# Performance work log

Hardware: AMD Instinct MI355X
Metric: run time of the kernel (lower is better)

## Reference

```python
import jax, jax.numpy as jnp
import numpy as np

N, E, H, L, G, MAX_Z = 100000, 1600000, 128, 3, 1024, 1000
BN_EPS = 1e-5

def setup_inputs() -> dict:
    key = jax.random.key(0)
    ks = jax.random.split(key, 16)
    z = jax.random.randint(ks[0], (N,), 0, MAX_Z)
    edge_index = jax.random.randint(ks[1], (2, E), 0, N)
    batch = jnp.sort(jax.random.randint(ks[2], (N,), 0, G))
    s = 1.0 / np.sqrt(H)
    z_table = jax.random.normal(ks[3], (MAX_Z, H), jnp.float32)
    conv_W1 = jax.random.normal(ks[4], (L, H, H), jnp.float32) * s
    conv_b1 = jnp.zeros((L, H), jnp.float32)
    conv_W2 = jax.random.normal(ks[5], (L, H, H), jnp.float32) * s
    conv_b2 = jnp.zeros((L, H), jnp.float32)
    bn_gamma = jnp.ones((L, H), jnp.float32)
    bn_beta = jnp.zeros((L, H), jnp.float32)
    lin1_W = jax.random.normal(ks[6], (L * H, H), jnp.float32) / np.sqrt(L * H)
    lin1_b = jnp.zeros((H,), jnp.float32)
    lin2_W = jax.random.normal(ks[7], (H, 1), jnp.float32) * s
    lin2_b = jnp.zeros((1,), jnp.float32)
    return {"z": z, "edge_index": edge_index, "batch": batch,
            "z_table": z_table, "conv_W1": conv_W1, "conv_b1": conv_b1,
            "conv_W2": conv_W2, "conv_b2": conv_b2, "bn_gamma": bn_gamma,
            "bn_beta": bn_beta, "lin1_W": lin1_W, "lin1_b": lin1_b,
            "lin2_W": lin2_W, "lin2_b": lin2_b}

def _gin_layer(x, src, dst, W1, b1, W2, b2, gamma, beta):
    # GIN sum aggregation: (1+eps)*x_i + sum_{j->i} x_j  (eps=0)
    agg = x + jax.ops.segment_sum(x[src], dst, num_segments=N)
    h = jax.nn.relu(agg @ W1 + b1)
    h = jax.nn.relu(h @ W2 + b2)
    # BatchNorm1d (training-mode batch statistics over nodes)
    mu = jnp.mean(h, axis=0)
    var = jnp.mean(jnp.square(h - mu), axis=0)
    return gamma * (h - mu) * jax.lax.rsqrt(var + BN_EPS) + beta

def reference(z, edge_index, batch, z_table, conv_W1, conv_b1, conv_W2,
              conv_b2, bn_gamma, bn_beta, lin1_W, lin1_b, lin2_W, lin2_b):
    src, dst = edge_index[0], edge_index[1]
    x = z_table[z]                      # [N, H]
    xs = []
    for l in range(L):
        x = _gin_layer(x, src, dst, conv_W1[l], conv_b1[l], conv_W2[l],
                       conv_b2[l], bn_gamma[l], bn_beta[l])
        xs.append(x)
    feat = jnp.concatenate(xs, axis=1)  # [N, L*H] (jk=True)
    sums = jax.ops.segment_sum(feat, batch, num_segments=G)
    cnt = jax.ops.segment_sum(jnp.ones((N,), feat.dtype), batch, num_segments=G)
    pooled = sums / jnp.maximum(cnt, 1.0)[:, None]   # global_mean_pool [G, L*H]
    h = jax.nn.relu(pooled @ lin1_W + lin1_b)
    # dropout inactive (eval mode)
    return h @ lin2_W + lin2_b          # [G, 1]
```

## Files before the change

### kernel.cpp

```cpp
#include <hip/hip_runtime.h>

#define NN 100000
#define NE 1600000
#define HD 128
#define NL 3
#define NG 1024
#define BN_EPS 1e-5f
#define SCAN_CHUNK 1024

static inline int cdiv(int a, int b) { return (a + b - 1) / b; }

__global__ __launch_bounds__(256) void embed_kernel(const int* __restrict__ z,
    const float* __restrict__ table, float* __restrict__ x) {
  int t = blockIdx.x * 256 + threadIdx.x;
  if (t >= NN * 32) return;
  int row = t >> 5, c4 = (t & 31) << 2;
  int zi = z[row];
  *(float4*)(x + (size_t)row * HD + c4) =
      *(const float4*)(table + (size_t)zi * HD + c4);
}

__global__ __launch_bounds__(256) void zero_counts_kernel(int* __restrict__ cnt) {
  int t = blockIdx.x * 256 + threadIdx.x;
  if (t < NN) cnt[t] = 0;
}

__global__ __launch_bounds__(256) void hist_kernel(const int* __restrict__ dstI,
    int* __restrict__ cnt) {
  int e = blockIdx.x * 256 + threadIdx.x;
  if (e < NE) atomicAdd(&cnt[dstI[e]], 1);
}

__global__ __launch_bounds__(256) void scan_block_kernel(const int* __restrict__ cnt,
    int* __restrict__ rowptr, int* __restrict__ bsums) {
  __shared__ int sh[SCAN_CHUNK];
  __shared__ int ts[256];
  int base = blockIdx.x * SCAN_CHUNK;
  for (int i = threadIdx.x; i < SCAN_CHUNK; i += 256)
    sh[i] = (base + i < NN) ? cnt[base + i] : 0;
  __syncthreads();
  int t4 = threadIdx.x * 4;
  int a0 = sh[t4], a1 = sh[t4 + 1], a2 = sh[t4 + 2], a3 = sh[t4 + 3];
  int tsum = a0 + a1 + a2 + a3;
  ts[threadIdx.x] = tsum;
  __syncthreads();
  for (int off = 1; off < 256; off <<= 1) {
    int v = ts[threadIdx.x];
    int u = (threadIdx.x >= off) ? ts[threadIdx.x - off] : 0;
    __syncthreads();
    ts[threadIdx.x] = v + u;
    __syncthreads();
  }
  int texcl = ts[threadIdx.x] - tsum;
  sh[t4] = texcl;
  sh[t4 + 1] = texcl + a0;
  sh[t4 + 2] = texcl + a0 + a1;
  sh[t4 + 3] = texcl + a0 + a1 + a2;
  __syncthreads();
  for (int i = threadIdx.x; i < SCAN_CHUNK; i += 256) {
    int g = base + i;
    if (g < NN) rowptr[g] = sh[i];
  }
  if (threadIdx.x == 255) bsums[blockIdx.x] = ts[255];
}

__global__ void scan_bsums_kernel(int* __restrict__ bsums, int nb) {
  if (threadIdx.x == 0) {
    int run = 0;
    for (int i = 0; i < nb; ++i) { int v = bsums[i]; bsums[i] = run; run += v; }
  }
}

__global__ __launch_bounds__(256) void scan_add_kernel(int* __restrict__ rowptr,
    const int* __restrict__ bsums, int* __restrict__ fill_off) {
  int t = blockIdx.x * 256 + threadIdx.x;
  if (t < NN) {
    int v = rowptr[t] + bsums[t / SCAN_CHUNK];
    rowptr[t] = v;
    fill_off[t] = v;
  }
  if (t == 0) rowptr[NN] = NE;
}

__global__ __launch_bounds__(256) void fill_kernel(const int* __restrict__ srcI,
    const int* __restrict__ dstI, int* __restrict__ fill_off, int* __restrict__ esrc) {
  int e = blockIdx.x * 256 + threadIdx.x;
  if (e >= NE) return;
  int d = dstI[e];
  int pos = atomicAdd(&fill_off[d], 1);
  esrc[pos] = srcI[e];
}

__global__ __launch_bounds__(256) void agg_kernel(const int* __restrict__ rowptr,
    const int* __restrict__ esrc, const float* __restrict__ xin, int xstride,
    float* __restrict__ agg) {
  int n = blockIdx.x * 4 + (threadIdx.x >> 6);
  if (n >= NN) return;
  int lane = threadIdx.x & 63;
  int lo = rowptr[n], hi = rowptr[n + 1];
  int deg = hi - lo;
  float2 acc = *(const float2*)(xin + (size_t)n * xstride + lane * 2);

  for (int base = 0; base < deg; base += 64) {
    int cnt = deg - base; if (cnt > 64) cnt = 64;
    int idx = (base + lane < deg) ? esrc[lo + base + lane] : 0;
    int j = 0;
    for (; j + 4 <= cnt; j += 4) {
      int s0 = __shfl(idx, j, 64);
      int s1 = __shfl(idx, j + 1, 64);
      int s2 = __shfl(idx, j + 2, 64);
      int s3 = __shfl(idx, j + 3, 64);
      float2 v0 = *(const float2*)(xin + (size_t)s0 * xstride + lane * 2);
      float2 v1 = *(const float2*)(xin + (size_t)s1 * xstride + lane * 2);
      float2 v2 = *(const float2*)(xin + (size_t)s2 * xstride + lane * 2);
      float2 v3 = *(const float2*)(xin + (size_t)s3 * xstride + lane * 2);
      acc.x += v0.x + v1.x + v2.x + v3.x;
      acc.y += v0.y + v1.y + v2.y + v3.y;
    }
    for (; j < cnt; ++j) {
      int s = __shfl(idx, j, 64);
      float2 v = *(const float2*)(xin + (size_t)s * xstride + lane * 2);
      acc.x += v.x; acc.y += v.y;
    }
  }
  *(float2*)(agg + (size_t)n * HD + lane * 2) = acc;
}

template <int STATS>
__global__ __launch_bounds__(256) void gemm_relu_kernel_t(
    const float* __restrict__ A, const float* __restrict__ B,
    const float* __restrict__ bias, float* __restrict__ C, int M,
    float* __restrict__ gsums) {
  __shared__ float As[128][65];
  __shared__ float Bs[32][128];
  __shared__ float csum[256];
  const int tid = threadIdx.x;
  const int row0 = blockIdx.x * 64;

  if (STATS) { csum[tid] = 0.f; }

  #pragma unroll
  for (int i = 0; i < 8; ++i) {
    int f = tid + i * 256;
    int row = f >> 5;
    int kq = (f & 31) << 2;
    int gr = row0 + row;
    float4 v = make_float4(0.f, 0.f, 0.f, 0.f);
    if (gr < M) v = *(const float4*)(A + (size_t)gr * HD + kq);
    As[kq + 0][row] = v.x; As[kq + 1][row] = v.y;
    As[kq + 2][row] = v.z; As[kq + 3][row] = v.w;
  }

  const int colbase = (tid & 15) << 2;
  const int rowbase = (tid >> 4) << 2;
  float acc[4][8] = {};

  for (int kc = 0; kc < 4; ++kc) {
    __syncthreads();
    #pragma unroll
    for (int i = 0; i < 4; ++i) {
      int f = tid + i * 256;
      int k = f >> 5;
      int c4 = (f & 31) << 2;
      *(float4*)(&Bs[k][c4]) = *(const float4*)(B + (size_t)(kc * 32 + k) * HD + c4);
    }
    __syncthreads();
    #pragma unroll
    for (int k = 0; k < 32; ++k) {
      const int kk = kc * 32 + k;
      float a0 = As[kk][rowbase + 0];
      float a1 = As[kk][rowbase + 1];
      float a2 = As[kk][rowbase + 2];
      float a3 = As[kk][rowbase + 3];
      float4 bl = *(const float4*)(&Bs[k][colbase]);
      float4 bh = *(const float4*)(&Bs[k][colbase + 64]);
      acc[0][0] += a0 * bl.x; acc[0][1] += a0 * bl.y; acc[0][2] += a0 * bl.z; acc[0][3] += a0 * bl.w;
      acc[0][4] += a0 * bh.x; acc[0][5] += a0 * bh.y; acc[0][6] += a0 * bh.z; acc[0][7] += a0 * bh.w;
      acc[1][0] += a1 * bl.x; acc[1][1] += a1 * bl.y; acc[1][2] += a1 * bl.z; acc[1][3] += a1 * bl.w;
      acc[1][4] += a1 * bh.x; acc[1][5] += a1 * bh.y; acc[1][6] += a1 * bh.z; acc[1][7] += a1 * bh.w;
      acc[2][0] += a2 * bl.x; acc[2][1] += a2 * bl.y; acc[2][2] += a2 * bl.z; acc[2][3] += a2 * bl.w;
      acc[2][4] += a2 * bh.x; acc[2][5] += a2 * bh.y; acc[2][6] += a2 * bh.z; acc[2][7] += a2 * bh.w;
      acc[3][0] += a3 * bl.x; acc[3][1] += a3 * bl.y; acc[3][2] += a3 * bl.z; acc[3][3] += a3 * bl.w;
      acc[3][4] += a3 * bh.x; acc[3][5] += a3 * bh.y; acc[3][6] += a3 * bh.z; acc[3][7] += a3 * bh.w;
    }
  }

  float4 bvl = *(const float4*)(bias + colbase);
  float4 bvh = *(const float4*)(bias + colbase + 64);
  float ps[8] = {}, pq[8] = {};
  #pragma unroll
  for (int r = 0; r < 4; ++r) {
    int gr = row0 + rowbase + r;
    if (gr < M) {
      float4 o;
      o.x = fmaxf(acc[r][0] + bvl.x, 0.f);
      o.y = fmaxf(acc[r][1] + bvl.y, 0.f);
      o.z = fmaxf(acc[r][2] + bvl.z, 0.f);
      o.w = fmaxf(acc[r][3] + bvl.w, 0.f);
      *(float4*)(C + (size_t)gr * HD + colbase) = o;
      if (STATS) {
        ps[0] += o.x; ps[1] += o.y; ps[2] += o.z; ps[3] += o.w;
        pq[0] += o.x * o.x; pq[1] += o.y * o.y; pq[2] += o.z * o.z; pq[3] += o.w * o.w;
      }
      o.x = fmaxf(acc[r][4] + bvh.x, 0.f);
      o.y = fmaxf(acc[r][5] + bvh.y, 0.f);
      o.z = fmaxf(acc[r][6] + bvh.z, 0.f);
      o.w = fmaxf(acc[r][7] + bvh.w, 0.f);
      *(float4*)(C + (size_t)gr * HD + colbase + 64) = o;
      if (STATS) {
        ps[4] += o.x; ps[5] += o.y; ps[6] += o.z; ps[7] += o.w;
        pq[4] += o.x * o.x; pq[5] += o.y * o.y; pq[6] += o.z * o.z; pq[7] += o.w * o.w;
      }
    }
  }

  if (STATS) {
    __syncthreads();
    #pragma unroll
    for (int c = 0; c < 4; ++c) {
      atomicAdd(&csum[colbase + c], ps[c]);
      atomicAdd(&csum[128 + colbase + c], pq[c]);
      atomicAdd(&csum[colbase + 64 + c], ps[4 + c]);
      atomicAdd(&csum[128 + colbase + 64 + c], pq[4 + c]);
    }
    __syncthreads();
    if (tid < 128) {
      atomicAdd(&gsums[tid], csum[tid]);
      atomicAdd(&gsums[HD + tid], csum[128 + tid]);
    }
  }
}

__global__ void zero_kernel(float* p) { p[threadIdx.x] = 0.f; }

__global__ void bn_finalize_kernel(const float* __restrict__ sums,
    const float* __restrict__ gamma, const float* __restrict__ beta,
    float* __restrict__ ss) {
  int c = threadIdx.x;
  float mu = sums[c] * (1.f / NN);
  float var = sums[HD + c] * (1.f / NN) - mu * mu;
  float sc = gamma[c] * rsqrtf(var + BN_EPS);
  ss[c] = sc;
  ss[HD + c] = beta[c] - mu * sc;
}

__global__ __launch_bounds__(256) void bn_apply_kernel(const float* __restrict__ h,
    const float* __restrict__ ss, float* __restrict__ featl) {
  int t = blockIdx.x * 256 + threadIdx.x;
  if (t >= NN * 32) return;
  int row = t >> 5, c4 = (t & 31) << 2;
  float4 v = *(const float4*)(h + (size_t)row * HD + c4);
  float4 sc = *(const float4*)(ss + c4);
  float4 sh = *(const float4*)(ss + HD + c4);
  float4 o;
  o.x = v.x * sc.x + sh.x;
  o.y = v.y * sc.y + sh.y;
  o.z = v.z * sc.z + sh.z;
  o.w = v.w * sc.w + sh.w;
  *(float4*)(featl + (size_t)row * (NL * HD) + c4) = o;
}

__device__ __forceinline__ int lbound(const int* __restrict__ b, int val) {
  int lo = 0, hi = NN;
  while (lo < hi) { int m = (lo + hi) >> 1; if (b[m] < val) lo = m + 1; else hi = m; }
  return lo;
}

__global__ __launch_bounds__(384) void pool_kernel(const int* __restrict__ batch,
    const float* __restrict__ feat, float* __restrict__ pooled) {
  int g = blockIdx.x;
  int lo = lbound(batch, g), hi = lbound(batch, g + 1);
  float s = 0.f;
  for (int r = lo; r < hi; ++r) s += feat[(size_t)r * (NL * HD) + threadIdx.x];
  float inv = 1.f / (float)max(hi - lo, 1);
  pooled[(size_t)g * (NL * HD) + threadIdx.x] = s * inv;
}

__global__ __launch_bounds__(128) void mlp_kernel(const float* __restrict__ pooled,
    const float* __restrict__ W1, const float* __restrict__ b1,
    const float* __restrict__ W2, const float* __restrict__ b2,
    float* __restrict__ out) {
  int g = blockIdx.x, c = threadIdx.x;
  const float* p = pooled + (size_t)g * (NL * HD);
  float acc = b1[c];
  #pragma unroll 4
  for (int k = 0; k < NL * HD; ++k) acc = fmaf(p[k], W1[(size_t)k * HD + c], acc);
  acc = fmaxf(acc, 0.f);
  float prod = acc * W2[c];
  #pragma unroll
  for (int off = 32; off > 0; off >>= 1) prod += __shfl_xor(prod, off, 64);
  __shared__ float part[2];
  if ((c & 63) == 0) part[c >> 6] = prod;
  __syncthreads();
  if (c == 0) out[g] = part[0] + part[1] + b2[0];
}

extern "C" void kernel_launch(void* const* d_in, const int* in_sizes, int n_in,
                              void* d_out, int out_size, void* d_ws, size_t ws_size,
                              hipStream_t stream) {
  (void)in_sizes; (void)n_in; (void)out_size; (void)ws_size;
  const int*   z     = (const int*)d_in[0];
  const int*   ei    = (const int*)d_in[1];
  const int*   batch = (const int*)d_in[2];
  const float* ztab  = (const float*)d_in[3];
  const float* W1    = (const float*)d_in[4];
  const float* b1    = (const float*)d_in[5];
  const float* W2    = (const float*)d_in[6];
  const float* b2    = (const float*)d_in[7];
  const float* gamma = (const float*)d_in[8];
  const float* beta  = (const float*)d_in[9];
  const float* l1W   = (const float*)d_in[10];
  const float* l1b   = (const float*)d_in[11];
  const float* l2W   = (const float*)d_in[12];
  const float* l2b   = (const float*)d_in[13];
  float* out = (float*)d_out;

  char* w = (char*)d_ws;
  float* bufA   = (float*)w; w += (size_t)NN * HD * 4;
  float* bufB   = (float*)w; w += (size_t)NN * HD * 4;
  float* feat   = (float*)w; w += (size_t)NN * (NL * HD) * 4;
  float* pooled = (float*)w; w += (size_t)NG * (NL * HD) * 4;
  float* sums   = (float*)w; w += 256 * 4;
  float* sshift = (float*)w; w += 256 * 4;
  int*   rowptr = (int*)w;   w += (size_t)(NN + 1) * 4;
  int*   counts = (int*)w;   w += (size_t)NN * 4;
  int*   filloff= (int*)w;   w += (size_t)NN * 4;
  int*   esrc   = (int*)w;   w += (size_t)NE * 4;
  int*   bsums  = (int*)w;   w += (size_t)cdiv(NN, SCAN_CHUNK) * 4;

  const int* srcI = ei;
  const int* dstI = ei + NE;

  dim3 blk(256);
  const int g_nh = cdiv(NN * 32, 256);
  const int g_nn = cdiv(NN, 256);
  const int g_ne = cdiv(NE, 256);
  const int nb_scan = cdiv(NN, SCAN_CHUNK);

  zero_counts_kernel<<<g_nn, blk, 0, stream>>>(counts);
  hist_kernel<<<g_ne, blk, 0, stream>>>(dstI, counts);
  scan_block_kernel<<<nb_scan, blk, 0, stream>>>(counts, rowptr, bsums);
  scan_bsums_kernel<<<1, 64, 0, stream>>>(bsums, nb_scan);
  scan_add_kernel<<<g_nn, blk, 0, stream>>>(rowptr, bsums, filloff);
  fill_kernel<<<g_ne, blk, 0, stream>>>(srcI, dstI, filloff, esrc);

  embed_kernel<<<g_nh, blk, 0, stream>>>(z, ztab, bufA);

  for (int l = 0; l < NL; ++l) {
    const float* xin;
    int xstride;
    if (l == 0) { xin = bufA; xstride = HD; }
    else        { xin = feat + (l - 1) * HD; xstride = NL * HD; }
    float* aggbuf = (l & 1) ? bufA : bufB;
    float* tmpbuf = (l & 1) ? bufB : bufA;

    agg_kernel<<<cdiv(NN, 4), blk, 0, stream>>>(rowptr, esrc, xin, xstride, aggbuf);
    gemm_relu_kernel_t<0><<<cdiv(NN, 64), blk, 0, stream>>>(aggbuf,
        W1 + (size_t)l * HD * HD, b1 + l * HD, tmpbuf, NN, nullptr);
    zero_kernel<<<1, 256, 0, stream>>>(sums);
    gemm_relu_kernel_t<1><<<cdiv(NN, 64), blk, 0, stream>>>(tmpbuf,
        W2 + (size_t)l * HD * HD, b2 + l * HD, aggbuf, NN, sums);
    bn_finalize_kernel<<<1, 128, 0, stream>>>(sums, gamma + l * HD, beta + l * HD, sshift);
    bn_apply_kernel<<<g_nh, blk, 0, stream>>>(aggbuf, sshift, feat + l * HD);
  }

  pool_kernel<<<NG, 384, 0, stream>>>(batch, feat, pooled);
  mlp_kernel<<<NG, 128, 0, stream>>>(pooled, l1W, l1b, l2W, l2b, out);
}
```

Measured before the change: 1.285 ms.

## Gather layer-0 neighbors directly from embedding table and accumulate BN stats in double

Drops the embedding materialization kernel. For layer 0 the aggregation now gathers rows straight from the small z_table, using per-edge z indices precomputed during CSR fill and stored in a reused buffer. The small table stays cache-resident, which should cut the random-gather traffic of the first aggregation. It also switches the BatchNorm sum and sum-of-squares accumulators to double-precision atomics for numerical stability, which could add some atomic cost.

```diff
diff --git a/kernel.cpp b/kernel.cpp
--- a/kernel.cpp
+++ b/kernel.cpp
@@ -9,16 +9,6 @@
 #define SCAN_CHUNK 1024
 
 static inline int cdiv(int a, int b) { return (a + b - 1) / b; }
-
-__global__ __launch_bounds__(256) void embed_kernel(const int* __restrict__ z,
-    const float* __restrict__ table, float* __restrict__ x) {
-  int t = blockIdx.x * 256 + threadIdx.x;
-  if (t >= NN * 32) return;
-  int row = t >> 5, c4 = (t & 31) << 2;
-  int zi = z[row];
-  *(float4*)(x + (size_t)row * HD + c4) =
-      *(const float4*)(table + (size_t)zi * HD + c4);
-}
 
 __global__ __launch_bounds__(256) void zero_counts_kernel(int* __restrict__ cnt) {
   int t = blockIdx.x * 256 + threadIdx.x;
@@ -83,43 +73,47 @@
 }
 
 __global__ __launch_bounds__(256) void fill_kernel(const int* __restrict__ srcI,
-    const int* __restrict__ dstI, int* __restrict__ fill_off, int* __restrict__ esrc) {
+    const int* __restrict__ dstI, const int* __restrict__ z,
+    int* __restrict__ fill_off, int* __restrict__ esrc, int* __restrict__ esrcz) {
   int e = blockIdx.x * 256 + threadIdx.x;
   if (e >= NE) return;
+  int s = srcI[e];
   int d = dstI[e];
   int pos = atomicAdd(&fill_off[d], 1);
-  esrc[pos] = srcI[e];
+  esrc[pos] = s;
+  esrcz[pos] = z[s];
 }
 
 __global__ __launch_bounds__(256) void agg_kernel(const int* __restrict__ rowptr,
-    const int* __restrict__ esrc, const float* __restrict__ xin, int xstride,
-    float* __restrict__ agg) {
+    const int* __restrict__ eidx, const float* __restrict__ xsrc, int xstride,
+    const int* __restrict__ selfz, float* __restrict__ agg) {
   int n = blockIdx.x * 4 + (threadIdx.x >> 6);
   if (n >= NN) return;
   int lane = threadIdx.x & 63;
   int lo = rowptr[n], hi = rowptr[n + 1];
   int deg = hi - lo;
-  float2 acc = *(const float2*)(xin + (size_t)n * xstride + lane * 2);
+  int selfrow = selfz ? selfz[n] : n;
+  float2 acc = *(const float2*)(xsrc + (size_t)selfrow * xstride + lane * 2);
 
   for (int base = 0; base < deg; base += 64) {
     int cnt = deg - base; if (cnt > 64) cnt = 64;
-    int idx = (base + lane < deg) ? esrc[lo + base + lane] : 0;
+    int idx = (base + lane < deg) ? eidx[lo + base + lane] : 0;
     int j = 0;
     for (; j + 4 <= cnt; j += 4) {
       int s0 = __shfl(idx, j, 64);
       int s1 = __shfl(idx, j + 1, 64);
       int s2 = __shfl(idx, j + 2, 64);
       int s3 = __shfl(idx, j + 3, 64);
-      float2 v0 = *(const float2*)(xin + (size_t)s0 * xstride + lane * 2);
-      float2 v1 = *(const float2*)(xin + (size_t)s1 * xstride + lane * 2);
-      float2 v2 = *(const float2*)(xin + (size_t)s2 * xstride + lane * 2);
-      float2 v3 = *(const float2*)(xin + (size_t)s3 * xstride + lane * 2);
+      float2 v0 = *(const float2*)(xsrc + (size_t)s0 * xstride + lane * 2);
+      float2 v1 = *(const float2*)(xsrc + (size_t)s1 * xstride + lane * 2);
+      float2 v2 = *(const float2*)(xsrc + (size_t)s2 * xstride + lane * 2);
+      float2 v3 = *(const float2*)(xsrc + (size_t)s3 * xstride + lane * 2);
       acc.x += v0.x + v1.x + v2.x + v3.x;
       acc.y += v0.y + v1.y + v2.y + v3.y;
     }
     for (; j < cnt; ++j) {
       int s = __shfl(idx, j, 64);
-      float2 v = *(const float2*)(xin + (size_t)s * xstride + lane * 2);
+      float2 v = *(const float2*)(xsrc + (size_t)s * xstride + lane * 2);
       acc.x += v.x; acc.y += v.y;
     }
   }
@@ -130,7 +124,7 @@
 __global__ __launch_bounds__(256) void gemm_relu_kernel_t(
     const float* __restrict__ A, const float* __restrict__ B,
     const float* __restrict__ bias, float* __restrict__ C, int M,
-    float* __restrict__ gsums) {
+    double* __restrict__ gsums) {
   __shared__ float As[128][65];
   __shared__ float Bs[32][128];
   __shared__ float csum[256];
@@ -225,23 +219,23 @@
     }
     __syncthreads();
     if (tid < 128) {
-      atomicAdd(&gsums[tid], csum[tid]);
-      atomicAdd(&gsums[HD + tid], csum[128 + tid]);
-    }
-  }
-}
-
-__global__ void zero_kernel(float* p) { p[threadIdx.x] = 0.f; }
-
-__global__ void bn_finalize_kernel(const float* __restrict__ sums,
+      atomicAdd(&gsums[tid], (double)csum[tid]);
+      atomicAdd(&gsums[HD + tid], (double)csum[128 + tid]);
+    }
+  }
+}
+
+__global__ void zero_d_kernel(double* p) { p[threadIdx.x] = 0.0; }
+
+__global__ void bn_finalize_kernel(const double* __restrict__ sums,
     const float* __restrict__ gamma, const float* __restrict__ beta,
     float* __restrict__ ss) {
   int c = threadIdx.x;
-  float mu = sums[c] * (1.f / NN);
-  float var = sums[HD + c] * (1.f / NN) - mu * mu;
-  float sc = gamma[c] * rsqrtf(var + BN_EPS);
+  double mu = sums[c] * (1.0 / NN);
+  double var = sums[HD + c] * (1.0 / NN) - mu * mu;
+  float sc = gamma[c] * (float)(1.0 / sqrt(var + (double)BN_EPS));
   ss[c] = sc;
-  ss[HD + c] = beta[c] - mu * sc;
+  ss[HD + c] = beta[c] - (float)mu * sc;
 }
 
 __global__ __launch_bounds__(256) void bn_apply_kernel(const float* __restrict__ h,
@@ -316,17 +310,18 @@
   float* out = (float*)d_out;
 
   char* w = (char*)d_ws;
-  float* bufA   = (float*)w; w += (size_t)NN * HD * 4;
-  float* bufB   = (float*)w; w += (size_t)NN * HD * 4;
-  float* feat   = (float*)w; w += (size_t)NN * (NL * HD) * 4;
-  float* pooled = (float*)w; w += (size_t)NG * (NL * HD) * 4;
-  float* sums   = (float*)w; w += 256 * 4;
-  float* sshift = (float*)w; w += 256 * 4;
-  int*   rowptr = (int*)w;   w += (size_t)(NN + 1) * 4;
-  int*   counts = (int*)w;   w += (size_t)NN * 4;
-  int*   filloff= (int*)w;   w += (size_t)NN * 4;
-  int*   esrc   = (int*)w;   w += (size_t)NE * 4;
-  int*   bsums  = (int*)w;   w += (size_t)cdiv(NN, SCAN_CHUNK) * 4;
+  float*  bufA   = (float*)w;  w += (size_t)NN * HD * 4;
+  float*  bufB   = (float*)w;  w += (size_t)NN * HD * 4;
+  float*  feat   = (float*)w;  w += (size_t)NN * (NL * HD) * 4;
+  float*  pooled = (float*)w;  w += (size_t)NG * (NL * HD) * 4;
+  double* sums   = (double*)w; w += 256 * 8;
+  float*  sshift = (float*)w;  w += 256 * 4;
+  int*    rowptr = (int*)w;    w += (size_t)(NN + 1) * 4;
+  int*    counts = (int*)w;    w += (size_t)NN * 4;
+  int*    filloff= (int*)w;    w += (size_t)NN * 4;
+  int*    esrc   = (int*)w;    w += (size_t)NE * 4;
+  int*    bsums  = (int*)w;    w += (size_t)cdiv(NN, SCAN_CHUNK) * 4;
+  int* esrcz = (int*)bufA;
 
   const int* srcI = ei;
   const int* dstI = ei + NE;
@@ -342,22 +337,21 @@
   scan_block_kernel<<<nb_scan, blk, 0, stream>>>(counts, rowptr, bsums);
   scan_bsums_kernel<<<1, 64, 0, stream>>>(bsums, nb_scan);
   scan_add_kernel<<<g_nn, blk, 0, stream>>>(rowptr, bsums, filloff);
-  fill_kernel<<<g_ne, blk, 0, stream>>>(srcI, dstI, filloff, esrc);
-
-  embed_kernel<<<g_nh, blk, 0, stream>>>(z, ztab, bufA);
+  fill_kernel<<<g_ne, blk, 0, stream>>>(srcI, dstI, z, filloff, esrc, esrcz);
 
   for (int l = 0; l < NL; ++l) {
-    const float* xin;
-    int xstride;
-    if (l == 0) { xin = bufA; xstride = HD; }
-    else        { xin = feat + (l - 1) * HD; xstride = NL * HD; }
     float* aggbuf = (l & 1) ? bufA : bufB;
     float* tmpbuf = (l & 1) ? bufB : bufA;
 
-    agg_kernel<<<cdiv(NN, 4), blk, 0, stream>>>(rowptr, esrc, xin, xstride, aggbuf);
+    if (l == 0) {
+      agg_kernel<<<cdiv(NN, 4), blk, 0, stream>>>(rowptr, esrcz, ztab, HD, z, aggbuf);
+    } else {
+      agg_kernel<<<cdiv(NN, 4), blk, 0, stream>>>(rowptr, esrc,
+          feat + (l - 1) * HD, NL * HD, nullptr, aggbuf);
+    }
     gemm_relu_kernel_t<0><<<cdiv(NN, 64), blk, 0, stream>>>(aggbuf,
         W1 + (size_t)l * HD * HD, b1 + l * HD, tmpbuf, NN, nullptr);
-    zero_kernel<<<1, 256, 0, stream>>>(sums);
+    zero_d_kernel<<<1, 256, 0, stream>>>(sums);
     gemm_relu_kernel_t<1><<<cdiv(NN, 64), blk, 0, stream>>>(tmpbuf,
         W2 + (size_t)l * HD * HD, b2 + l * HD, aggbuf, NN, sums);
     bn_finalize_kernel<<<1, 128, 0, stream>>>(sums, gamma + l * HD, beta + l * HD, sshift);
```

Result: faster. 1.200 ms (-6.6%).
